# Performance work log

Measured on AMD Instinct MI355X. Metric: run time of the kernel, lower is better.

Reference implementation:

```python
import jax, jax.numpy as jnp
import numpy as np

B, C, H, W, CLASSES = 128, 30, 15, 15, 16
ROUTINGS = 3
IN_NUM_CAPS = 32 * 11 * 11  # 3872
IN_DIM, OUT_DIM = 8, 16


def squash(x, axis=-1):
    norm = jnp.linalg.norm(x, axis=axis, keepdims=True)
    scale = norm ** 2 / (1 + norm ** 2) / (norm + 1e-8)
    return scale * x


def conv2d(x, w, b):
    y = jax.lax.conv_general_dilated(x, w, (1, 1), 'VALID',
                                     dimension_numbers=('NCHW', 'OIHW', 'NCHW'))
    return y + b[None, :, None, None]


def setup_inputs() -> dict:
    key = jax.random.key(0)
    ks = jax.random.split(key, 12)
    x = jax.random.normal(ks[0], (B, C, H, W), jnp.float32)
    labels = jax.random.randint(ks[1], (B,), 0, CLASSES)
    y = jax.nn.one_hot(labels, CLASSES, dtype=jnp.float32)
    conv1_w = 0.05 * jax.random.normal(ks[2], (256, C, 3, 3), jnp.float32)
    conv1_b = jnp.zeros((256,), jnp.float32)
    bn_gamma = jnp.ones((256,), jnp.float32)
    bn_beta = jnp.zeros((256,), jnp.float32)
    conv2_w = 0.05 * jax.random.normal(ks[3], (256, 256, 3, 3), jnp.float32)
    conv2_b = jnp.zeros((256,), jnp.float32)
    caps_w = 0.01 * jax.random.normal(ks[4], (CLASSES, IN_NUM_CAPS, OUT_DIM, IN_DIM), jnp.float32)
    dec_w1 = 0.05 * jax.random.normal(ks[5], (OUT_DIM * CLASSES, 328), jnp.float32)
    dec_b1 = jnp.zeros((328,), jnp.float32)
    dec_w2 = 0.05 * jax.random.normal(ks[6], (328, 192), jnp.float32)
    dec_b2 = jnp.zeros((192,), jnp.float32)
    dec_w3 = 0.05 * jax.random.normal(ks[7], (192, C * H * W), jnp.float32)
    dec_b3 = jnp.zeros((C * H * W,), jnp.float32)
    return dict(x=x, y=y, conv1_w=conv1_w, conv1_b=conv1_b, bn_gamma=bn_gamma,
                bn_beta=bn_beta, conv2_w=conv2_w, conv2_b=conv2_b, caps_w=caps_w,
                dec_w1=dec_w1, dec_b1=dec_b1, dec_w2=dec_w2, dec_b2=dec_b2,
                dec_w3=dec_w3, dec_b3=dec_b3)


def reference(x, y, conv1_w, conv1_b, bn_gamma, bn_beta, conv2_w, conv2_b,
              caps_w, dec_w1, dec_b1, dec_w2, dec_b2, dec_w3, dec_b3):
    # conv stem: conv -> batchnorm (batch stats, train mode) -> relu
    h = conv2d(x, conv1_w, conv1_b)                        # [B,256,13,13]
    mean = h.mean(axis=(0, 2, 3), keepdims=True)
    var = h.var(axis=(0, 2, 3), keepdims=True)
    h = (h - mean) / jnp.sqrt(var + 1e-5)
    h = h * bn_gamma[None, :, None, None] + bn_beta[None, :, None, None]
    h = jax.nn.relu(h)

    # primary capsules
    p = conv2d(h, conv2_w, conv2_b)                        # [B,256,11,11]
    caps = squash(p.reshape(B, -1, IN_DIM))                # [B,3872,8]

    # dense capsule: prediction vectors + dynamic routing
    x_hat = jnp.einsum('onij,bnj->boni', caps_w, caps)     # [B,16,3872,16]
    x_hat_det = jax.lax.stop_gradient(x_hat)
    b_log = jnp.zeros(x_hat.shape[:3], x_hat.dtype)        # [B,16,3872]
    out = None
    for i in range(ROUTINGS):
        c = jax.nn.softmax(b_log, axis=1)
        xh = x_hat if i == ROUTINGS - 1 else x_hat_det
        out = squash(jnp.einsum('bon,bond->bod', c, xh))   # [B,16,16]
        if i < ROUTINGS - 1:
            b_log = b_log + jnp.einsum('bod,bond->bon', out, x_hat_det)

    length = jnp.linalg.norm(out, axis=-1)                 # [B,16]

    # decoder MLP on label-masked capsules
    masked = (out * y[:, :, None]).reshape(B, -1)          # [B,256]
    r = jax.nn.sigmoid(masked @ dec_w1 + dec_b1)
    r = jax.nn.sigmoid(r @ dec_w2 + dec_b2)
    recon = (r @ dec_w3 + dec_b3).reshape(B, C, H, W)
    return length, recon
```

## Files before the change

### kernel.cpp

```cpp
#include <hip/hip_runtime.h>
#include <hip/hip_bf16.h>

#define NB 128
#define CIN 30
#define HW 15
#define OC 256
#define H1 13
#define H2 11
#define NCAPS 3872
#define IND 8
#define OUTD 16
#define CLS 16
#define D1 328
#define D2 192
#define OUTPIX 6750
#define NSPLIT 121
#define NPB 32
#define RN 2
#define ROUNDS 16

typedef __attribute__((ext_vector_type(8))) short short8_t;
typedef __attribute__((ext_vector_type(4))) float f32x4;
typedef __attribute__((ext_vector_type(4))) unsigned int u32x4;

__device__ inline unsigned bf16rne(float f) {
  unsigned u = __builtin_bit_cast(unsigned, f);
  return (u + 0x7FFF + ((u >> 16) & 1)) >> 16;
}

#define BLO(u) __builtin_bit_cast(float, (unsigned)((u) << 16))
#define BHI(u) __builtin_bit_cast(float, (unsigned)((u) & 0xffff0000u))

__global__ __launch_bounds__(256) void pack_w1_k(const float* __restrict__ w,
    unsigned short* __restrict__ wpk1) {
  int tid = blockIdx.x * blockDim.x + threadIdx.x;
  int j = tid & 7;
  int oc = (tid >> 3) & 255;
  int kc = (tid >> 11) & 3;
  int tap = tid >> 13;
  int ic = kc * 8 + j;
  float v = (ic < CIN) ? w[((size_t)oc * CIN + ic) * 9 + tap] : 0.f;
  wpk1[tid] = (unsigned short)bf16rne(v);
}

__global__ __launch_bounds__(512, 1) void conv1_mfma_k(
    const float* __restrict__ x, const unsigned short* __restrict__ wpk1,
    const float* __restrict__ bias, float* __restrict__ h) {
  __shared__ char smem[128 * 176 * 4];
  unsigned* hs32 = (unsigned*)smem;
  int bid = blockIdx.x;
  int b = bid >> 1;
  int nh = bid & 1;
  int t = threadIdx.x;
  int l = t & 63;
  int wid = t >> 6;

  if (t < 225) {
    const float* xb = x + (size_t)b * (CIN * 225);
#pragma unroll
    for (int icp = 0; icp < 15; icp++) {
      unsigned u0 = bf16rne(xb[(2 * icp) * 225 + t]);
      unsigned u1 = bf16rne(xb[(2 * icp + 1) * 225 + t]);
      hs32[t * 18 + icp] = u0 | (u1 << 16);
    }
    hs32[t * 18 + 15] = 0;
  }
  __syncthreads();

  int row = l & 15, kc = l >> 4;
  int ocb = nh * 128 + wid * 16;

  int arow[11];
#pragma unroll
  for (int mf = 0; mf < 11; mf++) {
    int m = mf * 16 + row;
    int pix = 0;
    if (m < 169) { int oy = m / 13, ox = m - oy * 13; pix = oy * HW + ox; }
    arow[mf] = pix * 72 + kc * 16;
  }

  f32x4 acc[11];
#pragma unroll
  for (int mf = 0; mf < 11; mf++) acc[mf] = (f32x4){0.f, 0.f, 0.f, 0.f};

  const size_t lanebase = ((size_t)ocb + row) * 8;
  const char* lds_base = (const char*)smem;

#pragma unroll
  for (int tap = 0; tap < 9; tap++) {
    const int ky = tap / 3, kx = tap % 3;
    const int koff = (ky * HW + kx) * 72;
    short8_t bfr = *(const short8_t*)(wpk1 + (size_t)(tap * 4 + kc) * 2048 + lanebase);
#pragma unroll
    for (int mf = 0; mf < 11; mf++) {
      short8_t af = *(const short8_t*)(lds_base + arow[mf] + koff);
      acc[mf] = __builtin_amdgcn_mfma_f32_16x16x32_bf16(af, bfr, acc[mf], 0, 0, 0);
    }
  }

  __syncthreads();
  float* cl = (float*)smem;
  {
    int ocl = wid * 16 + row;
#pragma unroll
    for (int mf = 0; mf < 11; mf++) {
      int m0 = mf * 16 + kc * 4;
      *(f32x4*)&cl[ocl * 176 + m0] = acc[mf];
    }
  }
  __syncthreads();
  for (int idx = t; idx < 128 * 169; idx += 512) {
    int ocl = idx / 169;
    int m = idx - ocl * 169;
    int oc = nh * 128 + ocl;
    h[((size_t)b * 256 + oc) * 169 + m] = cl[ocl * 176 + m] + bias[oc];
  }
}

__global__ __launch_bounds__(256) void bn_stats_k(const float* __restrict__ h,
    float* __restrict__ mean, float* __restrict__ istd) {
  int c = blockIdx.x;
  int t = threadIdx.x;
  float s = 0.f, s2 = 0.f;
  const int per = H1 * H1;
  for (int i = t; i < NB * per; i += 256) {
    int b = i / per, pos = i - b * per;
    float v = h[(b * OC + c) * per + pos];
    s += v; s2 += v * v;
  }
  __shared__ float ls[256], ls2[256];
  ls[t] = s; ls2[t] = s2; __syncthreads();
  for (int off = 128; off > 0; off >>= 1) {
    if (t < off) { ls[t] += ls[t + off]; ls2[t] += ls2[t + off]; }
    __syncthreads();
  }
  if (t == 0) {
    const float inv_n = 1.0f / (NB * per);
    float m = ls[0] * inv_n;
    float v = ls2[0] * inv_n - m * m;
    mean[c] = m;
    istd[c] = rsqrtf(v + 1e-5f);
  }
}

__global__ __launch_bounds__(256) void bn_apply_k(float* __restrict__ h,
    const float* __restrict__ mean, const float* __restrict__ istd,
    const float* __restrict__ gamma, const float* __restrict__ beta) {
  int bc = blockIdx.x;
  int c = bc & 255;
  int t = threadIdx.x;
  if (t >= H1 * H1) return;
  float v = h[bc * (H1 * H1) + t];
  v = (v - mean[c]) * istd[c] * gamma[c] + beta[c];
  h[bc * (H1 * H1) + t] = fmaxf(v, 0.0f);
}

__global__ __launch_bounds__(256) void pack_w2_k(const float* __restrict__ w,
    unsigned short* __restrict__ wpk) {
  int tid = blockIdx.x * blockDim.x + threadIdx.x;
  int e = tid & 7;
  int oc = (tid >> 3) & 255;
  int icchunk = (tid >> 11) & 31;
  int kykx = tid >> 16;
  int ic = icchunk * 8 + e;
  wpk[tid] = (unsigned short)bf16rne(w[((size_t)oc * 256 + ic) * 9 + kykx]);
}

__global__ __launch_bounds__(512, 1) void conv2_mfma_k(
    const float* __restrict__ h, const unsigned short* __restrict__ wpk,
    const float* __restrict__ bias, float* __restrict__ p) {
  __shared__ char smem[169 * 544];
  unsigned* hs32 = (unsigned*)smem;
  int bid = blockIdx.x;
  int b = bid >> 1;
  int nh = bid & 1;
  int t = threadIdx.x;
  int l = t & 63, wid = t >> 6;

  {
    const float* hb = h + (size_t)b * 256 * 169;
    for (int icp = wid; icp < 128; icp += 8) {
      const float* s0 = hb + (size_t)icp * 2 * 169;
#pragma unroll
      for (int pb = 0; pb < 3; pb++) {
        int pix = pb * 64 + l;
        if (pix < 169) {
          unsigned u0 = bf16rne(s0[pix]);
          unsigned u1 = bf16rne(s0[169 + pix]);
          hs32[pix * 136 + icp] = u0 | (u1 << 16);
        }
      }
    }
  }
  __syncthreads();

  int wm = wid & 1;
  int wn = wid >> 1;
  int row = l & 15, kc = l >> 4;
  int ocb = nh * 128 + wn * 32;

  int abase[4];
#pragma unroll
  for (int mf = 0; mf < 4; mf++) {
    int m = wm * 64 + mf * 16 + row;
    int p0 = (m < 121) ? ((m / 11) * 13 + (m % 11)) : 0;
    abase[mf] = p0 * 544 + kc * 16;
  }

  f32x4 acc[4][2];
#pragma unroll
  for (int mf = 0; mf < 4; mf++)
#pragma unroll
    for (int nf = 0; nf < 2; nf++)
      acc[mf][nf] = (f32x4){0.f, 0.f, 0.f, 0.f};

  const size_t lanebase = ((size_t)kc * 256 + ocb + row) * 8;
  const char* lds_base = (const char*)smem;

  for (int ky = 0; ky < 3; ky++) {
    for (int kx = 0; kx < 3; kx++) {
      int r = ky * 3 + kx;
      int koff = (ky * 13 + kx) * 544;
#pragma unroll
      for (int ks = 0; ks < 8; ks++) {
        short8_t bfr[2];
#pragma unroll
        for (int nf = 0; nf < 2; nf++) {
          size_t idx = lanebase + (size_t)(r * 32 + ks * 4) * 2048 + nf * 128;
          bfr[nf] = *(const short8_t*)(wpk + idx);
        }
        short8_t af[4];
#pragma unroll
        for (int mf = 0; mf < 4; mf++)
          af[mf] = *(const short8_t*)(lds_base + (abase[mf] + koff + ks * 64));
#pragma unroll
        for (int mf = 0; mf < 4; mf++)
#pragma unroll
          for (int nf = 0; nf < 2; nf++)
            acc[mf][nf] = __builtin_amdgcn_mfma_f32_16x16x32_bf16(
                af[mf], bfr[nf], acc[mf][nf], 0, 0, 0);
      }
    }
  }

  __syncthreads();
  float* cl = (float*)smem;
#pragma unroll
  for (int nf = 0; nf < 2; nf++) {
    int ocl = wn * 32 + nf * 16 + row;
#pragma unroll
    for (int mf = 0; mf < 4; mf++) {
      int m0 = wm * 64 + mf * 16 + kc * 4;
      f32x4 v = acc[mf][nf];
      *(f32x4*)&cl[ocl * 132 + m0] = v;
    }
  }
  __syncthreads();
  for (int idx = t; idx < 128 * 128; idx += 512) {
    int ocl = idx >> 7, m = idx & 127;
    if (m < 121) {
      int oc = nh * 128 + ocl;
      p[((size_t)b * 256 + oc) * 121 + m] = cl[ocl * 132 + m] + bias[oc];
    }
  }
}

__global__ __launch_bounds__(256) void squash_caps_k(const float* __restrict__ p,
    float* __restrict__ caps) {
  int tid = blockIdx.x * blockDim.x + threadIdx.x;
  const int total = NB * NCAPS;
  if (tid >= total) return;
  const float4* src = (const float4*)(p + (size_t)tid * 8);
  float4 a = src[0], b4 = src[1];
  float n2 = a.x * a.x + a.y * a.y + a.z * a.z + a.w * a.w +
             b4.x * b4.x + b4.y * b4.y + b4.z * b4.z + b4.w * b4.w;
  float nrm = sqrtf(n2);
  float scale = n2 / (1.0f + n2) / (nrm + 1e-8f);
  a.x *= scale; a.y *= scale; a.z *= scale; a.w *= scale;
  b4.x *= scale; b4.y *= scale; b4.z *= scale; b4.w *= scale;
  float4* dst = (float4*)(caps + (size_t)tid * 8);
  dst[0] = a; dst[1] = b4;
}

__global__ __launch_bounds__(256) void pack_cw_k(const float* __restrict__ cw,
    unsigned short* __restrict__ Wp16) {
  int idx = blockIdx.x * blockDim.x + threadIdx.x;
  int i = idx & 15;
  int j = (idx >> 4) & 7;
  int o = (idx >> 7) & 15;
  int n = idx >> 11;
  Wp16[idx] = (unsigned short)bf16rne(cw[(((size_t)o * NCAPS + n) * 16 + i) * 8 + j]);
}

__global__ __launch_bounds__(256) void route_k(const float* __restrict__ caps,
    const unsigned short* __restrict__ Wp16, const float* __restrict__ osum,
    float* __restrict__ spart) {
  __shared__ unsigned short wl[2][RN * 2176];
  int id = blockIdx.x;
  int xcd = id & 7;
  int lin = (xcd < 4 ? xcd * 61 : 244 + (xcd - 4) * 60) + (id >> 3);
  int split = lin >> 2;
  int btile = lin & 3;
  int t = threadIdx.x;
  int o = t & 15;
  int bp = t >> 4;
  int b0 = btile * 32 + bp * 2;

  const float* opa = osum + (b0 * 16 + o) * 16;
  f32x4 oa0 = *(const f32x4*)(opa);
  f32x4 oa1 = *(const f32x4*)(opa + 4);
  f32x4 oa2 = *(const f32x4*)(opa + 8);
  f32x4 oa3 = *(const f32x4*)(opa + 12);
  const float* opb = opa + 256;
  f32x4 ob0 = *(const f32x4*)(opb);
  f32x4 ob1 = *(const f32x4*)(opb + 4);
  f32x4 ob2 = *(const f32x4*)(opb + 8);
  f32x4 ob3 = *(const f32x4*)(opb + 12);
  f32x4 sA0 = {0.f,0.f,0.f,0.f}, sA1 = {0.f,0.f,0.f,0.f};
  f32x4 sA2 = {0.f,0.f,0.f,0.f}, sA3 = {0.f,0.f,0.f,0.f};
  f32x4 sB0 = {0.f,0.f,0.f,0.f}, sB1 = {0.f,0.f,0.f,0.f};
  f32x4 sB2 = {0.f,0.f,0.f,0.f}, sB3 = {0.f,0.f,0.f,0.f};

  int nbeg = split * NPB;
  const u32x4* src = (const u32x4*)(Wp16 + (size_t)nbeg * 2048);

  int e0 = t, e1 = t + 256;
  int d0 = (e0 >> 8) * 2176 + ((e0 >> 4) & 15) * 136 + (e0 & 15) * 8;
  int d1 = (e1 >> 8) * 2176 + ((e1 >> 4) & 15) * 136 + (e1 & 15) * 8;

  {
    u32x4 v0 = src[e0], v1 = src[e1];
    *(u32x4*)&wl[0][d0] = v0;
    *(u32x4*)&wl[0][d1] = v1;
  }
  __syncthreads();

  for (int r = 0; r < ROUNDS; r++) {
    u32x4 nv0, nv1;
    if (r < ROUNDS - 1) {
      const u32x4* s2 = src + (r + 1) * 512;
      nv0 = s2[e0]; nv1 = s2[e1];
    }
    const unsigned short* wlb = wl[r & 1];
#pragma unroll
    for (int nl = 0; nl < RN; nl++) {
      int n = nbeg + r * RN + nl;
      const float4* cpa = (const float4*)(caps + ((size_t)b0 * NCAPS + n) * 8);
      const float4* cpb = (const float4*)(caps + ((size_t)(b0 + 1) * NCAPS + n) * 8);
      float4 cqa0 = cpa[0], cqa1 = cpa[1];
      float4 cqb0 = cpb[0], cqb1 = cpb[1];
      float caA[8] = {cqa0.x, cqa0.y, cqa0.z, cqa0.w, cqa1.x, cqa1.y, cqa1.z, cqa1.w};
      float caB[8] = {cqb0.x, cqb0.y, cqb0.z, cqb0.w, cqb1.x, cqb1.y, cqb1.z, cqb1.w};
      const unsigned short* wp = wlb + nl * 2176 + o * 136;
      f32x4 xa0 = {0.f,0.f,0.f,0.f}, xa1 = {0.f,0.f,0.f,0.f};
      f32x4 xa2 = {0.f,0.f,0.f,0.f}, xa3 = {0.f,0.f,0.f,0.f};
      f32x4 xb0 = {0.f,0.f,0.f,0.f}, xb1 = {0.f,0.f,0.f,0.f};
      f32x4 xb2 = {0.f,0.f,0.f,0.f}, xb3 = {0.f,0.f,0.f,0.f};
#pragma unroll
      for (int j = 0; j < 8; j++) {
        u32x4 wA = *(const u32x4*)(wp + j * 16);
        u32x4 wB = *(const u32x4*)(wp + j * 16 + 8);
        f32x4 w0 = {BLO(wA.x), BHI(wA.x), BLO(wA.y), BHI(wA.y)};
        f32x4 w1 = {BLO(wA.z), BHI(wA.z), BLO(wA.w), BHI(wA.w)};
        f32x4 w2 = {BLO(wB.x), BHI(wB.x), BLO(wB.y), BHI(wB.y)};
        f32x4 w3 = {BLO(wB.z), BHI(wB.z), BLO(wB.w), BHI(wB.w)};
        float cjA = caA[j], cjB = caB[j];
        xa0 += w0 * cjA; xa1 += w1 * cjA; xa2 += w2 * cjA; xa3 += w3 * cjA;
        xb0 += w0 * cjB; xb1 += w1 * cjB; xb2 += w2 * cjB; xb3 += w3 * cjB;
      }
      f32x4 pA = oa0 * xa0 + oa1 * xa1 + oa2 * xa2 + oa3 * xa3;
      f32x4 pB = ob0 * xb0 + ob1 * xb1 + ob2 * xb2 + ob3 * xb3;
      float blogA = (pA.x + pA.y) + (pA.z + pA.w);
      float blogB = (pB.x + pB.y) + (pB.z + pB.w);
      float eA = __expf(blogA);
      float eB = __expf(blogB);
      float ssA = eA, ssB = eB;
      ssA += __shfl_xor(ssA, 1); ssB += __shfl_xor(ssB, 1);
      ssA += __shfl_xor(ssA, 2); ssB += __shfl_xor(ssB, 2);
      ssA += __shfl_xor(ssA, 4); ssB += __shfl_xor(ssB, 4);
      ssA += __shfl_xor(ssA, 8); ssB += __shfl_xor(ssB, 8);
      float ccA = eA * __builtin_amdgcn_rcpf(ssA);
      float ccB = eB * __builtin_amdgcn_rcpf(ssB);
      sA0 += xa0 * ccA; sA1 += xa1 * ccA; sA2 += xa2 * ccA; sA3 += xa3 * ccA;
      sB0 += xb0 * ccB; sB1 += xb1 * ccB; sB2 += xb2 * ccB; sB3 += xb3 * ccB;
    }
    if (r < ROUNDS - 1) {
      unsigned short* dst = wl[(r + 1) & 1];
      *(u32x4*)&dst[d0] = nv0;
      *(u32x4*)&dst[d1] = nv1;
      __syncthreads();
    }
  }
  float* spA = spart + (((size_t)split * NB + b0) * 16 + o) * 16;
  *(f32x4*)spA = sA0; *(f32x4*)(spA + 4) = sA1;
  *(f32x4*)(spA + 8) = sA2; *(f32x4*)(spA + 12) = sA3;
  float* spB = spA + 256;
  *(f32x4*)spB = sB0; *(f32x4*)(spB + 4) = sB1;
  *(f32x4*)(spB + 8) = sB2; *(f32x4*)(spB + 12) = sB3;
}

__global__ __launch_bounds__(256) void combine_squash_k(const float* __restrict__ spart,
    float* __restrict__ osum, float* __restrict__ outbuf, const float* __restrict__ y,
    float* __restrict__ masked, float* __restrict__ length_out, int last) {
  int tid = blockIdx.x * blockDim.x + threadIdx.x;
  int i = tid & 15;
  int o = (tid >> 4) & 15;
  int b = tid >> 8;
  float s = 0.f;
  for (int k = 0; k < NSPLIT; k++) s += spart[k * 32768 + tid];
  float n2 = s * s;
#pragma unroll
  for (int d = 1; d < 16; d <<= 1) n2 += __shfl_xor(n2, d);
  float nrm = sqrtf(n2);
  float scale = n2 / (1.f + n2) / (nrm + 1e-8f);
  float ov = scale * s;
  outbuf[tid] = ov;
  osum[tid] += ov;
  if (last) {
    masked[tid] = ov * y[b * 16 + o];
    if (i == 0) length_out[b * 16 + o] = scale * nrm;
  }
}

__global__ __launch_bounds__(256) void dec1_k(const float* __restrict__ masked,
    const float* __restrict__ w1, const float* __restrict__ b1, float* __restrict__ r1) {
  int tid = blockIdx.x * blockDim.x + threadIdx.x;
  if (tid >= NB * D1) return;
  int j = tid % D1;
  int b = tid / D1;
  const float* mp = masked + b * 256;
  float acc = b1[j];
  for (int k = 0; k < 256; k++) acc += mp[k] * w1[k * D1 + j];
  r1[tid] = 1.f / (1.f + __expf(-acc));
}

__global__ __launch_bounds__(256) void dec2_k(const float* __restrict__ r1,
    const float* __restrict__ w2, const float* __restrict__ b2, float* __restrict__ r2) {
  int tid = blockIdx.x * blockDim.x + threadIdx.x;
  if (tid >= NB * D2) return;
  int j = tid % D2;
  int b = tid / D2;
  const float* rp = r1 + b * D1;
  float acc = b2[j];
  for (int k = 0; k < D1; k++) acc += rp[k] * w2[k * D2 + j];
  r2[tid] = 1.f / (1.f + __expf(-acc));
}

__global__ __launch_bounds__(256) void dec3_k(const float* __restrict__ r2,
    const float* __restrict__ w3, const float* __restrict__ b3, float* __restrict__ recon) {
  __shared__ float r2s[D2 * 64];
  int mt = blockIdx.x, bh = blockIdx.y;
  int t = threadIdx.x;
  int b0 = bh * 64;
  for (int idx = t; idx < D2 * 64; idx += 256) {
    int bb = idx / D2, k = idx - bb * D2;
    r2s[k * 64 + bb] = r2[(b0 + bb) * D2 + k];
  }
  __syncthreads();
  int moff = t & 63, bg = t >> 6;
  int m = mt * 64 + moff;
  if (m >= OUTPIX) return;
  float acc[16];
#pragma unroll
  for (int q = 0; q < 16; q++) acc[q] = 0.f;
  for (int k = 0; k < D2; k++) {
    float wv = w3[k * OUTPIX + m];
    const float4* r4 = (const float4*)&r2s[k * 64 + bg * 16];
#pragma unroll
    for (int v = 0; v < 4; v++) {
      float4 rv = r4[v];
      acc[v * 4 + 0] += wv * rv.x;
      acc[v * 4 + 1] += wv * rv.y;
      acc[v * 4 + 2] += wv * rv.z;
      acc[v * 4 + 3] += wv * rv.w;
    }
  }
  float bias = b3[m];
#pragma unroll
  for (int q = 0; q < 16; q++) {
    int b = b0 + bg * 16 + q;
    recon[(size_t)b * OUTPIX + m] = acc[q] + bias;
  }
}

extern "C" void kernel_launch(void* const* d_in, const int* in_sizes, int n_in,
                              void* d_out, int out_size, void* d_ws, size_t ws_size,
                              hipStream_t stream) {
  const float* x      = (const float*)d_in[0];
  const float* y      = (const float*)d_in[1];
  const float* conv1w = (const float*)d_in[2];
  const float* conv1b = (const float*)d_in[3];
  const float* gamma  = (const float*)d_in[4];
  const float* beta   = (const float*)d_in[5];
  const float* conv2w = (const float*)d_in[6];
  const float* conv2b = (const float*)d_in[7];
  const float* capsw  = (const float*)d_in[8];
  const float* w1     = (const float*)d_in[9];
  const float* b1     = (const float*)d_in[10];
  const float* w2     = (const float*)d_in[11];
  const float* b2     = (const float*)d_in[12];
  const float* w3     = (const float*)d_in[13];
  const float* b3     = (const float*)d_in[14];

  float* ws = (float*)d_ws;
  float* h      = ws;
  float* p      = h + 5537792;
  float* caps   = p + 3964928;
  float* mean   = caps + 3964928;
  float* istd   = mean + 256;
  float* osum   = istd + 256;
  float* spart  = osum + 32768;
  float* outb   = spart + 3964928;
  float* masked = outb + 32768;
  float* r1     = masked + 32768;
  float* r2     = r1 + 41984;
  unsigned short* wpk = (unsigned short*)(r2 + 24576);
  unsigned short* wpk1 = wpk + 589824;
  unsigned short* Wp16 = (unsigned short*)ws;

  float* length_out = (float*)d_out;
  float* recon      = (float*)d_out + 2048;

  pack_w1_k<<<73728 / 256, 256, 0, stream>>>(conv1w, wpk1);
  conv1_mfma_k<<<256, 512, 0, stream>>>(x, wpk1, conv1b, h);
  bn_stats_k<<<OC, 256, 0, stream>>>(h, mean, istd);
  bn_apply_k<<<NB * OC, 256, 0, stream>>>(h, mean, istd, gamma, beta);

  pack_w2_k<<<589824 / 256, 256, 0, stream>>>(conv2w, wpk);
  conv2_mfma_k<<<256, 512, 0, stream>>>(h, wpk, conv2b, p);

  {
    int total = NB * NCAPS;
    squash_caps_k<<<(total + 255) / 256, 256, 0, stream>>>(p, caps);
  }

  pack_cw_k<<<7929856 / 256, 256, 0, stream>>>(capsw, Wp16);

  hipMemsetAsync(osum, 0, 32768 * sizeof(float), stream);
  for (int it = 0; it < 3; ++it) {
    route_k<<<484, 256, 0, stream>>>(caps, Wp16, osum, spart);
    combine_squash_k<<<128, 256, 0, stream>>>(spart, osum, outb, y, masked,
                                              length_out, it == 2 ? 1 : 0);
  }

  dec1_k<<<(NB * D1 + 255) / 256, 256, 0, stream>>>(masked, w1, b1, r1);
  dec2_k<<<(NB * D2 + 255) / 256, 256, 0, stream>>>(r1, w2, b2, r2);
  dec3_k<<<dim3((OUTPIX + 63) / 64, 2), 256, 0, stream>>>(r2, w3, b3, recon);
}
```

Baseline: 397.8 us.

## Fuse BN stats into conv1, BN-apply into conv2 load, double routing splits

Per-(batch,channel) sums and sums of squares are now computed inside conv1 from shared memory, and a tiny finalize kernel reduces them. This replaces the full-tensor bn_stats and bn_apply passes. The normalize+ReLU is folded into conv2's input staging. Separately, routing now uses 242 splits of 16 capsules (968 blocks) with partials written to two buffers, one aliased onto the no-longer-needed p buffer, which raises parallelism but doubles the combine reduction length.

Measured after the change: 399.2 us. About the same (+0.4%).

```diff
diff --git a/kernel.cpp b/kernel.cpp
--- a/kernel.cpp
+++ b/kernel.cpp
@@ -14,10 +14,10 @@
 #define D1 328
 #define D2 192
 #define OUTPIX 6750
-#define NSPLIT 121
-#define NPB 32
+#define NSPLIT 242
+#define NPB 16
 #define RN 2
-#define ROUNDS 16
+#define ROUNDS 8
 
 typedef __attribute__((ext_vector_type(8))) short short8_t;
 typedef __attribute__((ext_vector_type(4))) float f32x4;
@@ -45,7 +45,8 @@
 
 __global__ __launch_bounds__(512, 1) void conv1_mfma_k(
     const float* __restrict__ x, const unsigned short* __restrict__ wpk1,
-    const float* __restrict__ bias, float* __restrict__ h) {
+    const float* __restrict__ bias, float* __restrict__ h,
+    float* __restrict__ hsum, float* __restrict__ hsum2) {
   __shared__ char smem[128 * 176 * 4];
   unsigned* hs32 = (unsigned*)smem;
   int bid = blockIdx.x;
@@ -115,44 +116,37 @@
     int oc = nh * 128 + ocl;
     h[((size_t)b * 256 + oc) * 169 + m] = cl[ocl * 176 + m] + bias[oc];
   }
-}
-
-__global__ __launch_bounds__(256) void bn_stats_k(const float* __restrict__ h,
-    float* __restrict__ mean, float* __restrict__ istd) {
-  int c = blockIdx.x;
-  int t = threadIdx.x;
+  {
+    int ocl = t >> 2, sub = t & 3;
+    float bs = bias[nh * 128 + ocl];
+    float s1 = 0.f, s2 = 0.f;
+    int m0 = sub * 43, m1 = m0 + 43; if (m1 > 169) m1 = 169;
+    for (int m = m0; m < m1; m++) {
+      float v = cl[ocl * 176 + m] + bs;
+      s1 += v; s2 += v * v;
+    }
+    s1 += __shfl_xor(s1, 1); s2 += __shfl_xor(s2, 1);
+    s1 += __shfl_xor(s1, 2); s2 += __shfl_xor(s2, 2);
+    if (sub == 0) {
+      hsum[b * 256 + nh * 128 + ocl] = s1;
+      hsum2[b * 256 + nh * 128 + ocl] = s2;
+    }
+  }
+}
+
+__global__ __launch_bounds__(128) void bn_finalize_k(const float* __restrict__ hsum,
+    const float* __restrict__ hsum2, float* __restrict__ mean, float* __restrict__ istd) {
+  int c = blockIdx.x * 128 + threadIdx.x;
   float s = 0.f, s2 = 0.f;
-  const int per = H1 * H1;
-  for (int i = t; i < NB * per; i += 256) {
-    int b = i / per, pos = i - b * per;
-    float v = h[(b * OC + c) * per + pos];
-    s += v; s2 += v * v;
-  }
-  __shared__ float ls[256], ls2[256];
-  ls[t] = s; ls2[t] = s2; __syncthreads();
-  for (int off = 128; off > 0; off >>= 1) {
-    if (t < off) { ls[t] += ls[t + off]; ls2[t] += ls2[t + off]; }
-    __syncthreads();
-  }
-  if (t == 0) {
-    const float inv_n = 1.0f / (NB * per);
-    float m = ls[0] * inv_n;
-    float v = ls2[0] * inv_n - m * m;
-    mean[c] = m;
-    istd[c] = rsqrtf(v + 1e-5f);
-  }
-}
-
-__global__ __launch_bounds__(256) void bn_apply_k(float* __restrict__ h,
-    const float* __restrict__ mean, const float* __restrict__ istd,
-    const float* __restrict__ gamma, const float* __restrict__ beta) {
-  int bc = blockIdx.x;
-  int c = bc & 255;
-  int t = threadIdx.x;
-  if (t >= H1 * H1) return;
-  float v = h[bc * (H1 * H1) + t];
-  v = (v - mean[c]) * istd[c] * gamma[c] + beta[c];
-  h[bc * (H1 * H1) + t] = fmaxf(v, 0.0f);
+  for (int b = 0; b < NB; b++) {
+    s += hsum[b * 256 + c];
+    s2 += hsum2[b * 256 + c];
+  }
+  const float inv_n = 1.0f / (NB * H1 * H1);
+  float m = s * inv_n;
+  float v = s2 * inv_n - m * m;
+  mean[c] = m;
+  istd[c] = rsqrtf(v + 1e-5f);
 }
 
 __global__ __launch_bounds__(256) void pack_w2_k(const float* __restrict__ w,
@@ -168,7 +162,9 @@
 
 __global__ __launch_bounds__(512, 1) void conv2_mfma_k(
     const float* __restrict__ h, const unsigned short* __restrict__ wpk,
-    const float* __restrict__ bias, float* __restrict__ p) {
+    const float* __restrict__ bias, float* __restrict__ p,
+    const float* __restrict__ mean, const float* __restrict__ istd,
+    const float* __restrict__ gamma, const float* __restrict__ beta) {
   __shared__ char smem[169 * 544];
   unsigned* hs32 = (unsigned*)smem;
   int bid = blockIdx.x;
@@ -181,13 +177,16 @@
     const float* hb = h + (size_t)b * 256 * 169;
     for (int icp = wid; icp < 128; icp += 8) {
       const float* s0 = hb + (size_t)icp * 2 * 169;
+      int c0i = icp * 2, c1i = icp * 2 + 1;
+      float a0 = istd[c0i] * gamma[c0i], sh0 = beta[c0i] - mean[c0i] * a0;
+      float a1 = istd[c1i] * gamma[c1i], sh1 = beta[c1i] - mean[c1i] * a1;
 #pragma unroll
       for (int pb = 0; pb < 3; pb++) {
         int pix = pb * 64 + l;
         if (pix < 169) {
-          unsigned u0 = bf16rne(s0[pix]);
-          unsigned u1 = bf16rne(s0[169 + pix]);
-          hs32[pix * 136 + icp] = u0 | (u1 << 16);
+          float v0 = fmaxf(fmaf(s0[pix], a0, sh0), 0.f);
+          float v1 = fmaxf(fmaf(s0[169 + pix], a1, sh1), 0.f);
+          hs32[pix * 136 + icp] = bf16rne(v0) | (bf16rne(v1) << 16);
         }
       }
     }
@@ -294,11 +293,11 @@
 
 __global__ __launch_bounds__(256) void route_k(const float* __restrict__ caps,
     const unsigned short* __restrict__ Wp16, const float* __restrict__ osum,
-    float* __restrict__ spart) {
+    float* __restrict__ spart0, float* __restrict__ spart1) {
   __shared__ unsigned short wl[2][RN * 2176];
   int id = blockIdx.x;
   int xcd = id & 7;
-  int lin = (xcd < 4 ? xcd * 61 : 244 + (xcd - 4) * 60) + (id >> 3);
+  int lin = xcd * 121 + (id >> 3);
   int split = lin >> 2;
   int btile = lin & 3;
   int t = threadIdx.x;
@@ -391,7 +390,9 @@
       __syncthreads();
     }
   }
-  float* spA = spart + (((size_t)split * NB + b0) * 16 + o) * 16;
+  float* base = (split < 121) ? (spart0 + ((size_t)split * NB + b0) * 256)
+                              : (spart1 + ((size_t)(split - 121) * NB + b0) * 256);
+  float* spA = base + o * 16;
   *(f32x4*)spA = sA0; *(f32x4*)(spA + 4) = sA1;
   *(f32x4*)(spA + 8) = sA2; *(f32x4*)(spA + 12) = sA3;
   float* spB = spA + 256;
@@ -399,15 +400,17 @@
   *(f32x4*)(spB + 8) = sB2; *(f32x4*)(spB + 12) = sB3;
 }
 
-__global__ __launch_bounds__(256) void combine_squash_k(const float* __restrict__ spart,
-    float* __restrict__ osum, float* __restrict__ outbuf, const float* __restrict__ y,
+__global__ __launch_bounds__(256) void combine_squash_k(const float* __restrict__ spart0,
+    const float* __restrict__ spart1, float* __restrict__ osum,
+    float* __restrict__ outbuf, const float* __restrict__ y,
     float* __restrict__ masked, float* __restrict__ length_out, int last) {
   int tid = blockIdx.x * blockDim.x + threadIdx.x;
   int i = tid & 15;
   int o = (tid >> 4) & 15;
   int b = tid >> 8;
   float s = 0.f;
-  for (int k = 0; k < NSPLIT; k++) s += spart[k * 32768 + tid];
+  for (int k = 0; k < 121; k++) s += spart0[(size_t)k * 32768 + tid];
+  for (int k = 0; k < 121; k++) s += spart1[(size_t)k * 32768 + tid];
   float n2 = s * s;
 #pragma unroll
   for (int d = 1; d < 16; d <<= 1) n2 += __shfl_xor(n2, d);
@@ -509,25 +512,27 @@
   float* mean   = caps + 3964928;
   float* istd   = mean + 256;
   float* osum   = istd + 256;
-  float* spart  = osum + 32768;
-  float* outb   = spart + 3964928;
+  float* spart0 = osum + 32768;
+  float* outb   = spart0 + 3964928;
   float* masked = outb + 32768;
   float* r1     = masked + 32768;
   float* r2     = r1 + 41984;
   unsigned short* wpk = (unsigned short*)(r2 + 24576);
   unsigned short* wpk1 = wpk + 589824;
   unsigned short* Wp16 = (unsigned short*)ws;
+  float* spart1 = p;
+  float* hsum  = spart0;
+  float* hsum2 = spart0 + 32768;
 
   float* length_out = (float*)d_out;
   float* recon      = (float*)d_out + 2048;
 
   pack_w1_k<<<73728 / 256, 256, 0, stream>>>(conv1w, wpk1);
-  conv1_mfma_k<<<256, 512, 0, stream>>>(x, wpk1, conv1b, h);
-  bn_stats_k<<<OC, 256, 0, stream>>>(h, mean, istd);
-  bn_apply_k<<<NB * OC, 256, 0, stream>>>(h, mean, istd, gamma, beta);
+  conv1_mfma_k<<<256, 512, 0, stream>>>(x, wpk1, conv1b, h, hsum, hsum2);
+  bn_finalize_k<<<2, 128, 0, stream>>>(hsum, hsum2, mean, istd);
 
   pack_w2_k<<<589824 / 256, 256, 0, stream>>>(conv2w, wpk);
-  conv2_mfma_k<<<256, 512, 0, stream>>>(h, wpk, conv2b, p);
+  conv2_mfma_k<<<256, 512, 0, stream>>>(h, wpk, conv2b, p, mean, istd, gamma, beta);
 
   {
     int total = NB * NCAPS;
@@ -538,8 +543,8 @@
 
   hipMemsetAsync(osum, 0, 32768 * sizeof(float), stream);
   for (int it = 0; it < 3; ++it) {
-    route_k<<<484, 256, 0, stream>>>(caps, Wp16, osum, spart);
-    combine_squash_k<<<128, 256, 0, stream>>>(spart, osum, outb, y, masked,
+    route_k<<<968, 256, 0, stream>>>(caps, Wp16, osum, spart0, spart1);
+    combine_squash_k<<<128, 256, 0, stream>>>(spart0, spart1, osum, outb, y, masked,
                                               length_out, it == 2 ? 1 : 0);
   }
 
```
